# Kernel optimization log

Measured on AMD Instinct MI355X. Metric: run time of the kernel, lower is better.

The kernel has to match this reference:

```python
import jax, jax.numpy as jnp
import numpy as np

N, E, G, D, H = 50000, 800000, 64, 64, 256  # nodes, edges, graphs, feat dim, mlp hidden


def _mlp(x, W1, b1, W2, b2):
    return jax.nn.relu(x @ W1 + b1) @ W2 + b2


def _param(key, fan_in, fan_out):
    return jax.random.normal(key, (fan_in, fan_out), dtype=jnp.float32) * (1.0 / np.sqrt(fan_in))


def setup_inputs() -> dict:
    key = jax.random.key(0)
    ks = jax.random.split(key, 16)
    inp = {
        "nf": jax.random.normal(ks[0], (N, D), dtype=jnp.float32),
        "ef": jax.random.normal(ks[1], (E, D), dtype=jnp.float32),
        "u": jax.random.normal(ks[2], (G, D), dtype=jnp.float32),
        "src": jax.random.randint(ks[3], (E,), 0, N, dtype=jnp.int32),
        "dst": jax.random.randint(ks[4], (E,), 0, N, dtype=jnp.int32),
        "node_gid": jnp.sort(jax.random.randint(ks[5], (N,), 0, G, dtype=jnp.int32)),
        "edge_gid": jnp.sort(jax.random.randint(ks[6], (E,), 0, G, dtype=jnp.int32)),
        # edge_model: in = De + 2*Dn + Du = 4D
        "eW1": _param(ks[7], 4 * D, H), "eb1": jnp.zeros((H,), jnp.float32),
        "eW2": _param(ks[8], H, D),     "eb2": jnp.zeros((D,), jnp.float32),
        # node_model: in = De + Dn + Du = 3D
        "nW1": _param(ks[9], 3 * D, H), "nb1": jnp.zeros((H,), jnp.float32),
        "nW2": _param(ks[10], H, D),    "nb2": jnp.zeros((D,), jnp.float32),
        # global_model: in = De + Dn + Du = 3D
        "gW1": _param(ks[11], 3 * D, H), "gb1": jnp.zeros((H,), jnp.float32),
        "gW2": _param(ks[12], H, D),     "gb2": jnp.zeros((D,), jnp.float32),
    }
    return inp


def reference(nf, ef, u, src, dst, node_gid, edge_gid,
              eW1, eb1, eW2, eb2, nW1, nb1, nW2, nb2, gW1, gb1, gW2, gb2):
    # --- edge update: cat([ef, src_nf, dst_nf, u_per_edge]) -> edge MLP ---
    u_e = u[edge_gid]                                   # [E, D] (repeat_interleave by batch_num_edges)
    em_in = jnp.concatenate([ef, nf[src], nf[dst], u_e], axis=-1)  # [E, 4D]
    ef_new = _mlp(em_in, eW1, eb1, eW2, eb2)            # [E, D]

    # --- message = copy_e, reduce = sum at destination nodes ---
    agg_m = jax.ops.segment_sum(ef_new, dst, num_segments=N)       # [N, D]

    # --- node update: cat([agg_m, nf, u_per_node]) -> node MLP ---
    u_n = u[node_gid]                                   # [N, D]
    nm_in = jnp.concatenate([agg_m, nf, u_n], axis=-1)  # [N, 3D]
    nf_new = _mlp(nm_in, nW1, nb1, nW2, nb2)            # [N, D]

    # --- global update: per-graph sum readouts of updated edge/node feats ---
    e_aggr = jax.ops.segment_sum(ef_new, edge_gid, num_segments=G)  # [G, D]
    n_aggr = jax.ops.segment_sum(nf_new, node_gid, num_segments=G)  # [G, D]
    gm_in = jnp.concatenate([e_aggr, n_aggr, u], axis=-1)           # [G, 3D]
    u_new = _mlp(gm_in, gW1, gb1, gW2, gb2)             # [G, D]

    return nf_new, ef_new, u_new
```

## Files before the change

### kernel.cpp

```cpp
#include <hip/hip_runtime.h>
#include <stdint.h>
#include <stddef.h>

#define NN 50000
#define EE 800000
#define GG 64
#define DD 64
#define HH 256

typedef float f32x4 __attribute__((ext_vector_type(4)));
typedef short s16x8 __attribute__((ext_vector_type(8)));
typedef short s16x4 __attribute__((ext_vector_type(4)));

__device__ __forceinline__ short f2bf(float f) {
    union { float f; unsigned u; } v; v.f = f;
    return (short)((v.u + 0x7FFFu + ((v.u >> 16) & 1u)) >> 16);
}

__device__ __forceinline__ s16x4 f2bf4(f32x4 v) {
    s16x4 h = { f2bf(v.x), f2bf(v.y), f2bf(v.z), f2bf(v.w) };
    return h;
}

__global__ void prep_weights(const float* __restrict__ eW1, const float* __restrict__ eW2,
                             const float* __restrict__ nW1, const float* __restrict__ nW2,
                             short* __restrict__ W1f, short* __restrict__ W2f,
                             short* __restrict__ NW1f, short* __restrict__ NW2f) {
    int idx = blockIdx.x * blockDim.x + threadIdx.x;
    int lane = (idx >> 3) & 63, j = idx & 7;
    int l15 = lane & 15, lq = lane >> 4;
    {
        int c = idx >> 9;
        int n = (c >> 5) * 64 + ((c >> 3) & 3) * 16 + l15;
        int k = lq * 8 + (c & 7) * 32 + j;
        W1f[idx] = f2bf(eW1[k * 256 + n]);
    }
    if (idx < 49152) {
        int c = idx >> 9;
        int w = c / 24, r = c - w * 24;
        int n = w * 64 + (r / 6) * 16 + l15;
        int k = lq * 8 + (r % 6) * 32 + j;
        NW1f[idx] = f2bf(nW1[k * 256 + n]);
    }
    if (idx < 16384) {
        int c = idx >> 9;
        int n = (c >> 3) * 16 + l15;
        int k = lq * 8 + (c & 7) * 32 + j;
        W2f[idx]  = f2bf(eW2[k * 64 + n]);
        NW2f[idx] = f2bf(nW2[k * 64 + n]);
    }
}

#define SA1 264
#define SAN 200

__global__ __launch_bounds__(256, 4) void edge_kernel(
    const float* __restrict__ nf, const float* __restrict__ ef, const float* __restrict__ u,
    const int* __restrict__ src, const int* __restrict__ dst, const int* __restrict__ egid,
    const short* __restrict__ W1f, const float* __restrict__ b1,
    const short* __restrict__ W2f, const float* __restrict__ b2,
    float* __restrict__ ef_new, float* __restrict__ agg_m, float* __restrict__ e_aggr)
{
    __shared__ __align__(16) short As[64 * SA1];
    __shared__ int dstS[64];
    __shared__ int gidS[64];
    __shared__ float redS[4][64];

    const int t = threadIdx.x;
    const int e0 = blockIdx.x * 64;
    const int wave = t >> 6, lane = t & 63;
    const int l15 = lane & 15, lq = lane >> 4;

    int idxv;
    if (wave == 0)      idxv = e0 + lane;
    else if (wave == 1) idxv = src[e0 + lane];
    else if (wave == 2) { idxv = dst[e0 + lane]; dstS[lane] = idxv; }
    else                { idxv = egid[e0 + lane]; gidS[lane] = idxv; }

    const float* segbase = (wave == 0) ? ef : (wave == 3) ? u : nf;

    {
        const int rsub = lane >> 4;
        const int c4 = (lane & 15) * 4;
        #pragma unroll
        for (int r = 0; r < 16; ++r) {
            const int row = r * 4 + rsub;
            const float* sp = segbase + (size_t)__shfl(idxv, row) * 64 + c4;
            f32x4 v = *(const f32x4*)sp;
            *(s16x4*)(As + row * SA1 + wave * 64 + c4) = f2bf4(v);
        }
    }
    __syncthreads();

    f32x4 acc[4][4] = {};
    const short* aB = As + l15 * SA1 + lq * 8;
    const short* bB = W1f + (size_t)(wave * 32) * 512 + lane * 8;
    #pragma unroll
    for (int kk = 0; kk < 8; ++kk) {
        s16x8 a[4], b[4];
        #pragma unroll
        for (int rt = 0; rt < 4; ++rt) a[rt] = *(const s16x8*)(aB + rt * 16 * SA1 + kk * 32);
        #pragma unroll
        for (int ct = 0; ct < 4; ++ct) b[ct] = *(const s16x8*)(bB + (ct * 8 + kk) * 512);
        #pragma unroll
        for (int rt = 0; rt < 4; ++rt)
            #pragma unroll
            for (int ct = 0; ct < 4; ++ct)
                acc[rt][ct] = __builtin_amdgcn_mfma_f32_16x16x32_bf16(a[rt], b[ct], acc[rt][ct], 0, 0, 0);
    }
    __syncthreads();

    #pragma unroll
    for (int ct = 0; ct < 4; ++ct) {
        int col = wave * 64 + ct * 16 + l15;
        float bb = b1[col];
        #pragma unroll
        for (int rt = 0; rt < 4; ++rt)
            #pragma unroll
            for (int r = 0; r < 4; ++r) {
                int rr = rt * 16 + lq * 4 + r;
                float v = acc[rt][ct][r] + bb;
                As[rr * SA1 + col] = f2bf(v > 0.f ? v : 0.f);
            }
    }
    __syncthreads();

    f32x4 acc2[4] = {};
    const short* aB2 = As + l15 * SA1 + lq * 8;
    const short* bB2 = W2f + (size_t)(wave * 8) * 512 + lane * 8;
    #pragma unroll
    for (int kk = 0; kk < 8; ++kk) {
        s16x8 b = *(const s16x8*)(bB2 + kk * 512);
        #pragma unroll
        for (int rt = 0; rt < 4; ++rt) {
            s16x8 a = *(const s16x8*)(aB2 + rt * 16 * SA1 + kk * 32);
            acc2[rt] = __builtin_amdgcn_mfma_f32_16x16x32_bf16(a, b, acc2[rt], 0, 0, 0);
        }
    }
    __syncthreads();

    float* Y2s = (float*)As;
    {
        const int colo = wave * 16 + l15;
        const float bo = b2[colo];
        #pragma unroll
        for (int rt = 0; rt < 4; ++rt)
            #pragma unroll
            for (int r = 0; r < 4; ++r) {
                int rr = rt * 16 + lq * 4 + r;
                Y2s[rr * 65 + colo] = acc2[rt][r] + bo;
            }
    }
    __syncthreads();

    const bool uni = (gidS[0] == gidS[63]);
    const int g0 = gidS[0];
    float ps = 0.f;
    #pragma unroll
    for (int r = 0; r < 16; ++r) {
        int row = wave * 16 + r;
        float v = Y2s[row * 65 + lane];
        __builtin_nontemporal_store(v, &ef_new[(size_t)(e0 + row) * 64 + lane]);
        atomicAdd(&agg_m[(size_t)dstS[row] * 64 + lane], v);
        ps += v;
    }
    if (uni) redS[wave][lane] = ps;
    __syncthreads();

    if (uni) {
        if (wave == 0) {
            float s = redS[0][lane] + redS[1][lane] + redS[2][lane] + redS[3][lane];
            atomicAdd(&e_aggr[g0 * 64 + lane], s);
        }
    } else if (t < 64) {
        float sum = 0.f; int g = gidS[0];
        for (int rr = 0; rr < 64; ++rr) {
            int gg = gidS[rr];
            if (gg != g) { atomicAdd(&e_aggr[g * 64 + t], sum); sum = 0.f; g = gg; }
            sum += Y2s[rr * 65 + t];
        }
        atomicAdd(&e_aggr[g * 64 + t], sum);
    }
}

__global__ __launch_bounds__(256, 4) void node_kernel(
    const float* __restrict__ nf, const float* __restrict__ u,
    const int* __restrict__ ngid, const float* __restrict__ agg_m,
    const short* __restrict__ W1f, const float* __restrict__ b1,
    const short* __restrict__ W2f, const float* __restrict__ b2,
    float* __restrict__ nf_new, float* __restrict__ n_aggr)
{
    __shared__ __align__(16) short As[64 * SA1];
    __shared__ int gidS[64];
    __shared__ float redS[4][64];

    const int t = threadIdx.x;
    const int n0 = blockIdx.x * 64;

    if (t < 64) gidS[t] = (n0 + t < NN) ? ngid[n0 + t] : -1;
    __syncthreads();

    #pragma unroll
    for (int itq = 0; itq < 4; ++itq) {
        int idx = itq * 256 + t;
        int row = idx >> 4;
        int c4 = (idx & 15) * 4;
        bool valid = (n0 + row) < NN;
        f32x4 va = {0.f, 0.f, 0.f, 0.f}, vb = va, vc = va;
        if (valid) {
            int g = gidS[row];
            va = *(const f32x4*)(agg_m + (size_t)(n0 + row) * 64 + c4);
            vb = *(const f32x4*)(nf + (size_t)(n0 + row) * 64 + c4);
            vc = *(const f32x4*)(u + (size_t)g * 64 + c4);
        }
        short* arow = As + row * SAN;
        *(s16x4*)(arow + c4)        = f2bf4(va);
        *(s16x4*)(arow + 64 + c4)   = f2bf4(vb);
        *(s16x4*)(arow + 128 + c4)  = f2bf4(vc);
    }
    __syncthreads();

    const int wave = t >> 6, lane = t & 63;
    const int l15 = lane & 15, lq = lane >> 4;

    f32x4 acc[4][4] = {};
    {
        const short* aB = As + l15 * SAN + lq * 8;
        const short* bB = W1f + (size_t)(wave * 24) * 512 + lane * 8;
        #pragma unroll
        for (int kk = 0; kk < 6; ++kk) {
            s16x8 a[4], b[4];
            #pragma unroll
            for (int rt = 0; rt < 4; ++rt) a[rt] = *(const s16x8*)(aB + rt * 16 * SAN + kk * 32);
            #pragma unroll
            for (int ct = 0; ct < 4; ++ct) b[ct] = *(const s16x8*)(bB + (ct * 6 + kk) * 512);
            #pragma unroll
            for (int rt = 0; rt < 4; ++rt)
                #pragma unroll
                for (int ct = 0; ct < 4; ++ct)
                    acc[rt][ct] = __builtin_amdgcn_mfma_f32_16x16x32_bf16(a[rt], b[ct], acc[rt][ct], 0, 0, 0);
        }
    }
    __syncthreads();

    #pragma unroll
    for (int ct = 0; ct < 4; ++ct) {
        int col = wave * 64 + ct * 16 + l15;
        float bb = b1[col];
        #pragma unroll
        for (int rt = 0; rt < 4; ++rt)
            #pragma unroll
            for (int r = 0; r < 4; ++r) {
                int rr = rt * 16 + lq * 4 + r;
                float v = acc[rt][ct][r] + bb;
                As[rr * SA1 + col] = f2bf(v > 0.f ? v : 0.f);
            }
    }
    __syncthreads();

    f32x4 acc2[4] = {};
    {
        const short* aB2 = As + l15 * SA1 + lq * 8;
        const short* bB2 = W2f + (size_t)(wave * 8) * 512 + lane * 8;
        #pragma unroll
        for (int kk = 0; kk < 8; ++kk) {
            s16x8 b = *(const s16x8*)(bB2 + kk * 512);
            #pragma unroll
            for (int rt = 0; rt < 4; ++rt) {
                s16x8 a = *(const s16x8*)(aB2 + rt * 16 * SA1 + kk * 32);
                acc2[rt] = __builtin_amdgcn_mfma_f32_16x16x32_bf16(a, b, acc2[rt], 0, 0, 0);
            }
        }
    }
    __syncthreads();

    float* Y2s = (float*)As;
    {
        const int colo = wave * 16 + l15;
        const float bo = b2[colo];
        #pragma unroll
        for (int rt = 0; rt < 4; ++rt)
            #pragma unroll
            for (int r = 0; r < 4; ++r) {
                int rr = rt * 16 + lq * 4 + r;
                float v = acc2[rt][r] + bo;
                Y2s[rr * 65 + colo] = ((n0 + rr) < NN) ? v : 0.f;
            }
    }
    __syncthreads();

    const bool uni = (gidS[0] == gidS[63]) && (gidS[0] >= 0);
    const int g0 = gidS[0];
    float ps = 0.f;
    #pragma unroll
    for (int r = 0; r < 16; ++r) {
        int row = wave * 16 + r;
        float v = Y2s[row * 65 + lane];
        if ((n0 + row) < NN) nf_new[(size_t)(n0 + row) * 64 + lane] = v;
        ps += v;
    }
    if (uni) redS[wave][lane] = ps;
    __syncthreads();

    if (uni) {
        if (wave == 0) {
            float s = redS[0][lane] + redS[1][lane] + redS[2][lane] + redS[3][lane];
            atomicAdd(&n_aggr[g0 * 64 + lane], s);
        }
    } else if (t < 64) {
        float sum = 0.f; int g = gidS[0];
        for (int rr = 0; rr < 64; ++rr) {
            int gg = gidS[rr];
            if (gg != g) {
                if (g >= 0) atomicAdd(&n_aggr[g * 64 + t], sum);
                sum = 0.f; g = gg;
            }
            sum += Y2s[rr * 65 + t];
        }
        if (g >= 0) atomicAdd(&n_aggr[g * 64 + t], sum);
    }
}

__global__ void global_kernel(const float* __restrict__ e_aggr, const float* __restrict__ n_aggr,
                              const float* __restrict__ u,
                              const float* __restrict__ gW1, const float* __restrict__ gb1,
                              const float* __restrict__ gW2, const float* __restrict__ gb2,
                              float* __restrict__ u_new)
{
    __shared__ float gin[192];
    __shared__ float hid[256];
    const int g = blockIdx.x, t = threadIdx.x;
    if (t < 64)       gin[t] = e_aggr[g * 64 + t];
    else if (t < 128) gin[t] = n_aggr[g * 64 + (t - 64)];
    else if (t < 192) gin[t] = u[g * 64 + (t - 128)];
    __syncthreads();
    float s = gb1[t];
    #pragma unroll 8
    for (int k = 0; k < 192; ++k) s += gin[k] * gW1[k * 256 + t];
    hid[t] = s > 0.f ? s : 0.f;
    __syncthreads();
    if (t < 64) {
        float o = gb2[t];
        #pragma unroll 8
        for (int k = 0; k < 256; ++k) o += hid[k] * gW2[k * 64 + t];
        u_new[g * 64 + t] = o;
    }
}

#define WS_AGGM_OFF   0u
#define WS_AGGM_BYTES (NN * 64u * 4u)
#define WS_EAGG_OFF   (WS_AGGM_OFF + WS_AGGM_BYTES)
#define WS_NAGG_OFF   (WS_EAGG_OFF + GG * 64u * 4u)
#define WS_ZERO_BYTES (WS_NAGG_OFF + GG * 64u * 4u)
#define WS_W1T_OFF    WS_ZERO_BYTES
#define WS_W2T_OFF    (WS_W1T_OFF + 65536u * 2u)
#define WS_NW1T_OFF   (WS_W2T_OFF + 16384u * 2u)
#define WS_NW2T_OFF   (WS_NW1T_OFF + 49152u * 2u)

extern "C" void kernel_launch(void* const* d_in, const int* in_sizes, int n_in,
                              void* d_out, int out_size, void* d_ws, size_t ws_size,
                              hipStream_t stream) {
    const float* nf  = (const float*)d_in[0];
    const float* ef  = (const float*)d_in[1];
    const float* u   = (const float*)d_in[2];
    const int* src   = (const int*)d_in[3];
    const int* dst   = (const int*)d_in[4];
    const int* ngid  = (const int*)d_in[5];
    const int* egid  = (const int*)d_in[6];
    const float* eW1 = (const float*)d_in[7];
    const float* eb1 = (const float*)d_in[8];
    const float* eW2 = (const float*)d_in[9];
    const float* eb2 = (const float*)d_in[10];
    const float* nW1 = (const float*)d_in[11];
    const float* nb1 = (const float*)d_in[12];
    const float* nW2 = (const float*)d_in[13];
    const float* nb2 = (const float*)d_in[14];
    const float* gW1 = (const float*)d_in[15];
    const float* gb1 = (const float*)d_in[16];
    const float* gW2 = (const float*)d_in[17];
    const float* gb2 = (const float*)d_in[18];

    float* out    = (float*)d_out;
    float* nf_new = out;
    float* ef_new = out + (size_t)NN * DD;
    float* u_new  = out + (size_t)(NN + EE) * DD;

    char* ws = (char*)d_ws;
    float* agg_m  = (float*)(ws + WS_AGGM_OFF);
    float* e_aggr = (float*)(ws + WS_EAGG_OFF);
    float* n_aggr = (float*)(ws + WS_NAGG_OFF);
    short* W1f    = (short*)(ws + WS_W1T_OFF);
    short* W2f    = (short*)(ws + WS_W2T_OFF);
    short* NW1f   = (short*)(ws + WS_NW1T_OFF);
    short* NW2f   = (short*)(ws + WS_NW2T_OFF);

    hipMemsetAsync(d_ws, 0, WS_ZERO_BYTES, stream);
    prep_weights<<<256, 256, 0, stream>>>(eW1, eW2, nW1, nW2, W1f, W2f, NW1f, NW2f);
    edge_kernel<<<EE / 64, 256, 0, stream>>>(nf, ef, u, src, dst, egid,
                                             W1f, eb1, W2f, eb2, ef_new, agg_m, e_aggr);
    node_kernel<<<(NN + 63) / 64, 256, 0, stream>>>(nf, u, ngid, agg_m,
                                                    NW1f, nb1, NW2f, nb2, nf_new, n_aggr);
    global_kernel<<<GG, 256, 0, stream>>>(e_aggr, n_aggr, u, gW1, gb1, gW2, gb2, u_new);
}
```

Before: 630.9 us.

## Write MLP outputs directly from MFMA accumulators and prefetch W2 fragments

Both edge and node kernels drop the shared-memory staging of the second GEMM output. Stores, agg_m atomics and per-graph sums are now issued straight from the MFMA accumulator registers, with a shuffle reduction over the quad lanes, which removes two barriers and the LDS round trip. W2 fragments are loaded into registers before the ReLU/bias phase so their latency overlaps that work, and B loads are issued before A loads in the first GEMM. The risks are that stores become 16-float column segments per row rather than full 256-byte rows, so coalescing is worse, and non-uniform blocks issue many more e_aggr atomics.

Result: slower. 681.9 us (+8.1%).

```diff
diff --git a/kernel.cpp b/kernel.cpp
--- a/kernel.cpp
+++ b/kernel.cpp
@@ -64,7 +64,6 @@
     __shared__ __align__(16) short As[64 * SA1];
     __shared__ int dstS[64];
     __shared__ int gidS[64];
-    __shared__ float redS[4][64];
 
     const int t = threadIdx.x;
     const int e0 = blockIdx.x * 64;
@@ -97,11 +96,11 @@
     const short* bB = W1f + (size_t)(wave * 32) * 512 + lane * 8;
     #pragma unroll
     for (int kk = 0; kk < 8; ++kk) {
-        s16x8 a[4], b[4];
+        s16x8 b[4], a[4];
+        #pragma unroll
+        for (int ct = 0; ct < 4; ++ct) b[ct] = *(const s16x8*)(bB + (ct * 8 + kk) * 512);
         #pragma unroll
         for (int rt = 0; rt < 4; ++rt) a[rt] = *(const s16x8*)(aB + rt * 16 * SA1 + kk * 32);
-        #pragma unroll
-        for (int ct = 0; ct < 4; ++ct) b[ct] = *(const s16x8*)(bB + (ct * 8 + kk) * 512);
         #pragma unroll
         for (int rt = 0; rt < 4; ++rt)
             #pragma unroll
@@ -109,6 +108,13 @@
                 acc[rt][ct] = __builtin_amdgcn_mfma_f32_16x16x32_bf16(a[rt], b[ct], acc[rt][ct], 0, 0, 0);
     }
     __syncthreads();
+
+    s16x8 w2f[8];
+    {
+        const short* bB2 = W2f + (size_t)(wave * 8) * 512 + lane * 8;
+        #pragma unroll
+        for (int kk = 0; kk < 8; ++kk) w2f[kk] = *(const s16x8*)(bB2 + kk * 512);
+    }
 
     #pragma unroll
     for (int ct = 0; ct < 4; ++ct) {
@@ -127,59 +133,35 @@
 
     f32x4 acc2[4] = {};
     const short* aB2 = As + l15 * SA1 + lq * 8;
-    const short* bB2 = W2f + (size_t)(wave * 8) * 512 + lane * 8;
     #pragma unroll
     for (int kk = 0; kk < 8; ++kk) {
-        s16x8 b = *(const s16x8*)(bB2 + kk * 512);
         #pragma unroll
         for (int rt = 0; rt < 4; ++rt) {
             s16x8 a = *(const s16x8*)(aB2 + rt * 16 * SA1 + kk * 32);
-            acc2[rt] = __builtin_amdgcn_mfma_f32_16x16x32_bf16(a, b, acc2[rt], 0, 0, 0);
-        }
-    }
-    __syncthreads();
-
-    float* Y2s = (float*)As;
-    {
-        const int colo = wave * 16 + l15;
-        const float bo = b2[colo];
-        #pragma unroll
-        for (int rt = 0; rt < 4; ++rt)
-            #pragma unroll
-            for (int r = 0; r < 4; ++r) {
-                int rr = rt * 16 + lq * 4 + r;
-                Y2s[rr * 65 + colo] = acc2[rt][r] + bo;
-            }
-    }
-    __syncthreads();
-
+            acc2[rt] = __builtin_amdgcn_mfma_f32_16x16x32_bf16(a, w2f[kk], acc2[rt], 0, 0, 0);
+        }
+    }
+
+    const int colo = wave * 16 + l15;
+    const float bo = b2[colo];
     const bool uni = (gidS[0] == gidS[63]);
     const int g0 = gidS[0];
-    float ps = 0.f;
-    #pragma unroll
-    for (int r = 0; r < 16; ++r) {
-        int row = wave * 16 + r;
-        float v = Y2s[row * 65 + lane];
-        __builtin_nontemporal_store(v, &ef_new[(size_t)(e0 + row) * 64 + lane]);
-        atomicAdd(&agg_m[(size_t)dstS[row] * 64 + lane], v);
-        ps += v;
-    }
-    if (uni) redS[wave][lane] = ps;
-    __syncthreads();
-
+    float csum = 0.f;
+    #pragma unroll
+    for (int rt = 0; rt < 4; ++rt)
+        #pragma unroll
+        for (int r = 0; r < 4; ++r) {
+            int row = rt * 16 + lq * 4 + r;
+            float v = acc2[rt][r] + bo;
+            __builtin_nontemporal_store(v, &ef_new[(size_t)(e0 + row) * 64 + colo]);
+            atomicAdd(&agg_m[(size_t)dstS[row] * 64 + colo], v);
+            if (uni) csum += v;
+            else     atomicAdd(&e_aggr[gidS[row] * 64 + colo], v);
+        }
     if (uni) {
-        if (wave == 0) {
-            float s = redS[0][lane] + redS[1][lane] + redS[2][lane] + redS[3][lane];
-            atomicAdd(&e_aggr[g0 * 64 + lane], s);
-        }
-    } else if (t < 64) {
-        float sum = 0.f; int g = gidS[0];
-        for (int rr = 0; rr < 64; ++rr) {
-            int gg = gidS[rr];
-            if (gg != g) { atomicAdd(&e_aggr[g * 64 + t], sum); sum = 0.f; g = gg; }
-            sum += Y2s[rr * 65 + t];
-        }
-        atomicAdd(&e_aggr[g * 64 + t], sum);
+        csum += __shfl_xor(csum, 16);
+        csum += __shfl_xor(csum, 32);
+        if (lq == 0) atomicAdd(&e_aggr[g0 * 64 + colo], csum);
     }
 }
 
@@ -192,13 +174,11 @@
 {
     __shared__ __align__(16) short As[64 * SA1];
     __shared__ int gidS[64];
-    __shared__ float redS[4][64];
 
     const int t = threadIdx.x;
     const int n0 = blockIdx.x * 64;
 
     if (t < 64) gidS[t] = (n0 + t < NN) ? ngid[n0 + t] : -1;
-    __syncthreads();
 
     #pragma unroll
     for (int itq = 0; itq < 4; ++itq) {
@@ -208,7 +188,7 @@
         bool valid = (n0 + row) < NN;
         f32x4 va = {0.f, 0.f, 0.f, 0.f}, vb = va, vc = va;
         if (valid) {
-            int g = gidS[row];
+            int g = ngid[n0 + row];
             va = *(const f32x4*)(agg_m + (size_t)(n0 + row) * 64 + c4);
             vb = *(const f32x4*)(nf + (size_t)(n0 + row) * 64 + c4);
             vc = *(const f32x4*)(u + (size_t)g * 64 + c4);
@@ -229,11 +209,11 @@
         const short* bB = W1f + (size_t)(wave * 24) * 512 + lane * 8;
         #pragma unroll
         for (int kk = 0; kk < 6; ++kk) {
-            s16x8 a[4], b[4];
+            s16x8 b[4], a[4];
+            #pragma unroll
+            for (int ct = 0; ct < 4; ++ct) b[ct] = *(const s16x8*)(bB + (ct * 6 + kk) * 512);
             #pragma unroll
             for (int rt = 0; rt < 4; ++rt) a[rt] = *(const s16x8*)(aB + rt * 16 * SAN + kk * 32);
-            #pragma unroll
-            for (int ct = 0; ct < 4; ++ct) b[ct] = *(const s16x8*)(bB + (ct * 6 + kk) * 512);
             #pragma unroll
             for (int rt = 0; rt < 4; ++rt)
                 #pragma unroll
@@ -242,6 +222,13 @@
         }
     }
     __syncthreads();
+
+    s16x8 w2f[8];
+    {
+        const short* bB2 = W2f + (size_t)(wave * 8) * 512 + lane * 8;
+        #pragma unroll
+        for (int kk = 0; kk < 8; ++kk) w2f[kk] = *(const s16x8*)(bB2 + kk * 512);
+    }
 
     #pragma unroll
     for (int ct = 0; ct < 4; ++ct) {
@@ -261,63 +248,37 @@
     f32x4 acc2[4] = {};
     {
         const short* aB2 = As + l15 * SA1 + lq * 8;
-        const short* bB2 = W2f + (size_t)(wave * 8) * 512 + lane * 8;
         #pragma unroll
         for (int kk = 0; kk < 8; ++kk) {
-            s16x8 b = *(const s16x8*)(bB2 + kk * 512);
             #pragma unroll
             for (int rt = 0; rt < 4; ++rt) {
                 s16x8 a = *(const s16x8*)(aB2 + rt * 16 * SA1 + kk * 32);
-                acc2[rt] = __builtin_amdgcn_mfma_f32_16x16x32_bf16(a, b, acc2[rt], 0, 0, 0);
+                acc2[rt] = __builtin_amdgcn_mfma_f32_16x16x32_bf16(a, w2f[kk], acc2[rt], 0, 0, 0);
             }
         }
     }
-    __syncthreads();
-
-    float* Y2s = (float*)As;
-    {
-        const int colo = wave * 16 + l15;
-        const float bo = b2[colo];
-        #pragma unroll
-        for (int rt = 0; rt < 4; ++rt)
-            #pragma unroll
-            for (int r = 0; r < 4; ++r) {
-                int rr = rt * 16 + lq * 4 + r;
-                float v = acc2[rt][r] + bo;
-                Y2s[rr * 65 + colo] = ((n0 + rr) < NN) ? v : 0.f;
-            }
-    }
-    __syncthreads();
-
+
+    const int colo = wave * 16 + l15;
+    const float bo = b2[colo];
     const bool uni = (gidS[0] == gidS[63]) && (gidS[0] >= 0);
     const int g0 = gidS[0];
-    float ps = 0.f;
-    #pragma unroll
-    for (int r = 0; r < 16; ++r) {
-        int row = wave * 16 + r;
-        float v = Y2s[row * 65 + lane];
-        if ((n0 + row) < NN) nf_new[(size_t)(n0 + row) * 64 + lane] = v;
-        ps += v;
-    }
-    if (uni) redS[wave][lane] = ps;
-    __syncthreads();
-
+    float csum = 0.f;
+    #pragma unroll
+    for (int rt = 0; rt < 4; ++rt)
+        #pragma unroll
+        for (int r = 0; r < 4; ++r) {
+            int row = rt * 16 + lq * 4 + r;
+            if ((n0 + row) < NN) {
+                float v = acc2[rt][r] + bo;
+                nf_new[(size_t)(n0 + row) * 64 + colo] = v;
+                if (uni) csum += v;
+                else { int g = gidS[row]; if (g >= 0) atomicAdd(&n_aggr[g * 64 + colo], v); }
+            }
+        }
     if (uni) {
-        if (wave == 0) {
-            float s = redS[0][lane] + redS[1][lane] + redS[2][lane] + redS[3][lane];
-            atomicAdd(&n_aggr[g0 * 64 + lane], s);
-        }
-    } else if (t < 64) {
-        float sum = 0.f; int g = gidS[0];
-        for (int rr = 0; rr < 64; ++rr) {
-            int gg = gidS[rr];
-            if (gg != g) {
-                if (g >= 0) atomicAdd(&n_aggr[g * 64 + t], sum);
-                sum = 0.f; g = gg;
-            }
-            sum += Y2s[rr * 65 + t];
-        }
-        if (g >= 0) atomicAdd(&n_aggr[g * 64 + t], sum);
+        csum += __shfl_xor(csum, 16);
+        csum += __shfl_xor(csum, 32);
+        if (lq == 0) atomicAdd(&n_aggr[g0 * 64 + colo], csum);
     }
 }
 
```

## Swizzle edge LDS tile, drop padding, raise occupancy, prefetch W2 fragments

Applied to the files above, without the earlier changes.

Replaces the padded 264-stride LDS tile in the edge kernel with an unpadded 256-stride tile using an XOR swizzle to avoid bank conflicts. Shared arrays for dst and graph ids become per-lane registers read with shuffles, and the reduction buffer reuses the tile. Together these cut LDS per block so the launch bound can rise from 4 to 5 blocks per CU. Both kernels also load the second-layer weight fragments into registers before the ReLU/store phase so that global latency overlaps it, at the cost of extra registers under the tighter occupancy bound.

After: 878.5 us. 1.39x slower.

```diff
diff --git a/kernel.cpp b/kernel.cpp
--- a/kernel.cpp
+++ b/kernel.cpp
@@ -20,6 +20,10 @@
 __device__ __forceinline__ s16x4 f2bf4(f32x4 v) {
     s16x4 h = { f2bf(v.x), f2bf(v.y), f2bf(v.z), f2bf(v.w) };
     return h;
+}
+
+__device__ __forceinline__ int swz(int row, int s) {
+    return row * 256 + ((((s >> 3) ^ (row & 7)) << 3) | (s & 7));
 }
 
 __global__ void prep_weights(const float* __restrict__ eW1, const float* __restrict__ eW2,
@@ -54,28 +58,27 @@
 #define SA1 264
 #define SAN 200
 
-__global__ __launch_bounds__(256, 4) void edge_kernel(
+__global__ __launch_bounds__(256, 5) void edge_kernel(
     const float* __restrict__ nf, const float* __restrict__ ef, const float* __restrict__ u,
     const int* __restrict__ src, const int* __restrict__ dst, const int* __restrict__ egid,
     const short* __restrict__ W1f, const float* __restrict__ b1,
     const short* __restrict__ W2f, const float* __restrict__ b2,
     float* __restrict__ ef_new, float* __restrict__ agg_m, float* __restrict__ e_aggr)
 {
-    __shared__ __align__(16) short As[64 * SA1];
-    __shared__ int dstS[64];
-    __shared__ int gidS[64];
-    __shared__ float redS[4][64];
+    __shared__ __align__(16) short As[64 * 256];
 
     const int t = threadIdx.x;
     const int e0 = blockIdx.x * 64;
     const int wave = t >> 6, lane = t & 63;
     const int l15 = lane & 15, lq = lane >> 4;
 
+    const int dstv = dst[e0 + lane];
+    const int gidv = egid[e0 + lane];
     int idxv;
     if (wave == 0)      idxv = e0 + lane;
     else if (wave == 1) idxv = src[e0 + lane];
-    else if (wave == 2) { idxv = dst[e0 + lane]; dstS[lane] = idxv; }
-    else                { idxv = egid[e0 + lane]; gidS[lane] = idxv; }
+    else if (wave == 2) idxv = dstv;
+    else                idxv = gidv;
 
     const float* segbase = (wave == 0) ? ef : (wave == 3) ? u : nf;
 
@@ -87,19 +90,18 @@
             const int row = r * 4 + rsub;
             const float* sp = segbase + (size_t)__shfl(idxv, row) * 64 + c4;
             f32x4 v = *(const f32x4*)sp;
-            *(s16x4*)(As + row * SA1 + wave * 64 + c4) = f2bf4(v);
+            *(s16x4*)(As + swz(row, wave * 64 + c4)) = f2bf4(v);
         }
     }
     __syncthreads();
 
     f32x4 acc[4][4] = {};
-    const short* aB = As + l15 * SA1 + lq * 8;
     const short* bB = W1f + (size_t)(wave * 32) * 512 + lane * 8;
     #pragma unroll
     for (int kk = 0; kk < 8; ++kk) {
         s16x8 a[4], b[4];
         #pragma unroll
-        for (int rt = 0; rt < 4; ++rt) a[rt] = *(const s16x8*)(aB + rt * 16 * SA1 + kk * 32);
+        for (int rt = 0; rt < 4; ++rt) a[rt] = *(const s16x8*)(As + swz(rt * 16 + l15, lq * 8 + kk * 32));
         #pragma unroll
         for (int ct = 0; ct < 4; ++ct) b[ct] = *(const s16x8*)(bB + (ct * 8 + kk) * 512);
         #pragma unroll
@@ -109,6 +111,13 @@
                 acc[rt][ct] = __builtin_amdgcn_mfma_f32_16x16x32_bf16(a[rt], b[ct], acc[rt][ct], 0, 0, 0);
     }
     __syncthreads();
+
+    s16x8 w2f[8];
+    {
+        const short* bB2 = W2f + (size_t)(wave * 8) * 512 + lane * 8;
+        #pragma unroll
+        for (int kk = 0; kk < 8; ++kk) w2f[kk] = *(const s16x8*)(bB2 + kk * 512);
+    }
 
     #pragma unroll
     for (int ct = 0; ct < 4; ++ct) {
@@ -120,21 +129,18 @@
             for (int r = 0; r < 4; ++r) {
                 int rr = rt * 16 + lq * 4 + r;
                 float v = acc[rt][ct][r] + bb;
-                As[rr * SA1 + col] = f2bf(v > 0.f ? v : 0.f);
+                As[swz(rr, col)] = f2bf(v > 0.f ? v : 0.f);
             }
     }
     __syncthreads();
 
     f32x4 acc2[4] = {};
-    const short* aB2 = As + l15 * SA1 + lq * 8;
-    const short* bB2 = W2f + (size_t)(wave * 8) * 512 + lane * 8;
     #pragma unroll
     for (int kk = 0; kk < 8; ++kk) {
-        s16x8 b = *(const s16x8*)(bB2 + kk * 512);
         #pragma unroll
         for (int rt = 0; rt < 4; ++rt) {
-            s16x8 a = *(const s16x8*)(aB2 + rt * 16 * SA1 + kk * 32);
-            acc2[rt] = __builtin_amdgcn_mfma_f32_16x16x32_bf16(a, b, acc2[rt], 0, 0, 0);
+            s16x8 a = *(const s16x8*)(As + swz(rt * 16 + l15, lq * 8 + kk * 32));
+            acc2[rt] = __builtin_amdgcn_mfma_f32_16x16x32_bf16(a, w2f[kk], acc2[rt], 0, 0, 0);
         }
     }
     __syncthreads();
@@ -153,29 +159,30 @@
     }
     __syncthreads();
 
-    const bool uni = (gidS[0] == gidS[63]);
-    const int g0 = gidS[0];
+    const int g0 = __shfl(gidv, 0);
+    const bool uni = (g0 == __shfl(gidv, 63));
+    float* redS = (float*)As + 4224;
     float ps = 0.f;
     #pragma unroll
     for (int r = 0; r < 16; ++r) {
         int row = wave * 16 + r;
         float v = Y2s[row * 65 + lane];
         __builtin_nontemporal_store(v, &ef_new[(size_t)(e0 + row) * 64 + lane]);
-        atomicAdd(&agg_m[(size_t)dstS[row] * 64 + lane], v);
+        atomicAdd(&agg_m[(size_t)__shfl(dstv, row) * 64 + lane], v);
         ps += v;
     }
-    if (uni) redS[wave][lane] = ps;
+    if (uni) redS[wave * 64 + lane] = ps;
     __syncthreads();
 
     if (uni) {
         if (wave == 0) {
-            float s = redS[0][lane] + redS[1][lane] + redS[2][lane] + redS[3][lane];
+            float s = redS[lane] + redS[64 + lane] + redS[128 + lane] + redS[192 + lane];
             atomicAdd(&e_aggr[g0 * 64 + lane], s);
         }
     } else if (t < 64) {
-        float sum = 0.f; int g = gidS[0];
+        float sum = 0.f; int g = g0;
         for (int rr = 0; rr < 64; ++rr) {
-            int gg = gidS[rr];
+            int gg = __shfl(gidv, rr);
             if (gg != g) { atomicAdd(&e_aggr[g * 64 + t], sum); sum = 0.f; g = gg; }
             sum += Y2s[rr * 65 + t];
         }
@@ -243,6 +250,13 @@
     }
     __syncthreads();
 
+    s16x8 w2f[8];
+    {
+        const short* bB2 = W2f + (size_t)(wave * 8) * 512 + lane * 8;
+        #pragma unroll
+        for (int kk = 0; kk < 8; ++kk) w2f[kk] = *(const s16x8*)(bB2 + kk * 512);
+    }
+
     #pragma unroll
     for (int ct = 0; ct < 4; ++ct) {
         int col = wave * 64 + ct * 16 + l15;
@@ -261,14 +275,12 @@
     f32x4 acc2[4] = {};
     {
         const short* aB2 = As + l15 * SA1 + lq * 8;
-        const short* bB2 = W2f + (size_t)(wave * 8) * 512 + lane * 8;
         #pragma unroll
         for (int kk = 0; kk < 8; ++kk) {
-            s16x8 b = *(const s16x8*)(bB2 + kk * 512);
             #pragma unroll
             for (int rt = 0; rt < 4; ++rt) {
                 s16x8 a = *(const s16x8*)(aB2 + rt * 16 * SA1 + kk * 32);
-                acc2[rt] = __builtin_amdgcn_mfma_f32_16x16x32_bf16(a, b, acc2[rt], 0, 0, 0);
+                acc2[rt] = __builtin_amdgcn_mfma_f32_16x16x32_bf16(a, w2f[kk], acc2[rt], 0, 0, 0);
             }
         }
     }
```
